# Optimization experiments

Measured on AMD Instinct MI355X. Metric: run time of the kernel, lower is better.

Reference implementation:

```python
import jax, jax.numpy as jnp
import numpy as np

N_HEAD = 8
N_EMBD = 512
HEAD_DIM = N_EMBD // N_HEAD


def setup_inputs() -> dict:
    key = jax.random.key(0)
    ks = jax.random.split(key, 9)
    B, S, D = 2, 4096, N_EMBD
    scale = 1.0 / np.sqrt(D)
    x = jax.random.normal(ks[0], (B, S, D), dtype=jnp.float32)
    Wq = jax.random.normal(ks[1], (D, D), dtype=jnp.float32) * scale
    bq = jax.random.normal(ks[2], (D,), dtype=jnp.float32) * 0.01
    Wk = jax.random.normal(ks[3], (D, D), dtype=jnp.float32) * scale
    bk = jax.random.normal(ks[4], (D,), dtype=jnp.float32) * 0.01
    Wv = jax.random.normal(ks[5], (D, D), dtype=jnp.float32) * scale
    bv = jax.random.normal(ks[6], (D,), dtype=jnp.float32) * 0.01
    Wo = jax.random.normal(ks[7], (D, D), dtype=jnp.float32) * scale
    bo = jax.random.normal(ks[8], (D,), dtype=jnp.float32) * 0.01
    return {"x": x, "Wq": Wq, "bq": bq, "Wk": Wk, "bk": bk,
            "Wv": Wv, "bv": bv, "Wo": Wo, "bo": bo}


def reference(x, Wq, bq, Wk, bk, Wv, bv, Wo, bo):
    B, S, D = x.shape
    H, Hd = N_HEAD, HEAD_DIM
    q = (x @ Wq + bq).reshape(B, S, H, Hd)
    k = (x @ Wk + bk).reshape(B, S, H, Hd)
    v = (x @ Wv + bv).reshape(B, S, H, Hd)
    # scores: [B, H, S, S]
    scores = jnp.einsum('bqhd,bkhd->bhqk', q, k) / jnp.sqrt(jnp.asarray(Hd, x.dtype))
    attn = jax.nn.softmax(scores, axis=-1)
    out = jnp.einsum('bhqk,bkhd->bqhd', attn, v).reshape(B, S, D)
    return out @ Wo + bo
```

## Files before the change

kernel.cpp:

```cpp
#include <hip/hip_runtime.h>

#define DEV static __device__ __forceinline__

using f32x4 = __attribute__((ext_vector_type(4))) float;
using s16x8 = __attribute__((ext_vector_type(8))) short;

DEV unsigned short f2bf(float x) {
    unsigned int u = __float_as_uint(x);
    unsigned int r = (u + 0x7FFFu + ((u >> 16) & 1u)) >> 16;
    return (unsigned short)r;
}
DEV float bf2f(unsigned short u) {
    return __uint_as_float(((unsigned int)u) << 16);
}

DEV f32x4 mfma16(s16x8 a, s16x8 b, f32x4 c) {
    return __builtin_amdgcn_mfma_f32_16x16x32_bf16(a, b, c, 0, 0, 0);
}

DEV unsigned cvtpk_bf16(float a, float b) {
    unsigned r;
    asm volatile("v_cvt_pk_bf16_f32 %0, %1, %2" : "=v"(r) : "v"(a), "v"(b));
    return r;
}

DEV void gload16(const unsigned short* g, short* l) {
    __builtin_amdgcn_global_load_lds(
        (const __attribute__((address_space(1))) unsigned int*)g,
        (__attribute__((address_space(3))) unsigned int*)l, 16, 0, 0);
}

#define LOG2E 1.4426950408889634f

__global__ void k_split(const float* __restrict__ in, unsigned short* __restrict__ hi,
                        unsigned short* __restrict__ lo, int n4) {
    for (int i = blockIdx.x * blockDim.x + threadIdx.x; i < n4; i += gridDim.x * blockDim.x) {
        float4 v = ((const float4*)in)[i];
        ushort4 h, l;
        h.x = f2bf(v.x); l.x = f2bf(v.x - bf2f(h.x));
        h.y = f2bf(v.y); l.y = f2bf(v.y - bf2f(h.y));
        h.z = f2bf(v.z); l.z = f2bf(v.z - bf2f(h.z));
        h.w = f2bf(v.w); l.w = f2bf(v.w - bf2f(h.w));
        ((ushort4*)hi)[i] = h;
        ((ushort4*)lo)[i] = l;
    }
}

__global__ void k_wfuse(const float* __restrict__ Wq, const float* __restrict__ Wk,
                        const float* __restrict__ Wv, const float* __restrict__ Wo,
                        const float* __restrict__ bq, const float* __restrict__ bk,
                        const float* __restrict__ bv,
                        unsigned short* __restrict__ WBhi, unsigned short* __restrict__ WBlo,
                        unsigned short* __restrict__ Wothi, unsigned short* __restrict__ Wotlo,
                        float* __restrict__ bcat, float qs) {
    __shared__ float tile[64][65];
    int blk = blockIdx.x;
    if (blk >= 256) {
        int i = (blk - 256) * 256 + threadIdx.x;
        bcat[i] = (i < 512) ? bq[i] * qs : (i < 1024) ? bk[i - 512] : bv[i - 1024];
        return;
    }
    int wi = blk >> 6, sub = blk & 63;
    const float* W = (wi == 0) ? Wq : (wi == 1) ? Wk : (wi == 2) ? Wv : Wo;
    float scale = (wi == 0) ? qs : 1.0f;
    unsigned short* Thi = (wi < 3) ? WBhi + (size_t)wi * 512 * 512 : Wothi;
    unsigned short* Tlo = (wi < 3) ? WBlo + (size_t)wi * 512 * 512 : Wotlo;
    int bk0 = (sub >> 3) * 64, bn = (sub & 7) * 64;
    int t = threadIdx.x;
    int r = t >> 2, c4 = (t & 3) * 16;
#pragma unroll
    for (int j = 0; j < 16; j += 4) {
        float4 v = *(const float4*)&W[(size_t)(bk0 + r) * 512 + bn + c4 + j];
        tile[r][c4 + j + 0] = v.x; tile[r][c4 + j + 1] = v.y;
        tile[r][c4 + j + 2] = v.z; tile[r][c4 + j + 3] = v.w;
    }
    __syncthreads();
    int n = t >> 2, k4 = (t & 3) * 16;
#pragma unroll
    for (int j = 0; j < 16; ++j) {
        float x = tile[k4 + j][n] * scale;
        unsigned short h = f2bf(x);
        Thi[(size_t)(bn + n) * 512 + bk0 + k4 + j] = h;
        Tlo[(size_t)(bn + n) * 512 + bk0 + k4 + j] = f2bf(x - bf2f(h));
    }
}

template <int MODE>
__global__ __launch_bounds__(256, 2) void k_gemm2(
    const unsigned short* __restrict__ Ahi, const unsigned short* __restrict__ Alo,
    const unsigned short* __restrict__ Bhi, const unsigned short* __restrict__ Blo,
    const float* __restrict__ bias,
    unsigned short* __restrict__ Qh,
    unsigned short* __restrict__ Kh, unsigned short* __restrict__ Kl,
    unsigned short* __restrict__ Vt,
    float* __restrict__ Cf) {
    __shared__ short As[128 * 64];
    __shared__ short Bs[128 * 64];
    int t = threadIdx.x, lane = t & 63, w = t >> 6;
    int wr = w >> 1, wc = w & 1, lr = lane & 15, lg = lane >> 4;
    int bm = blockIdx.y * 128, bn = blockIdx.x * 128;
    f32x4 acc[4][4] = {};
    int srow = t >> 3;
    int sc = t & 7;
    int gcol = (sc ^ (srow & 7)) * 8;
    int axr = (lr & 7) * 8;
    for (int c = 0; c < 24; ++c) {
        int seg = c >> 3, kb = (c & 7) * 64;
        const unsigned short* Ap = (seg < 2) ? Ahi : Alo;
        const unsigned short* Bp = (seg == 1) ? Blo : Bhi;
        const unsigned short* ag = Ap + (size_t)(bm + srow) * 512 + kb + gcol;
        const unsigned short* bg = Bp + (size_t)(bn + srow) * 512 + kb + gcol;
#pragma unroll
        for (int ps = 0; ps < 4; ++ps) {
            gload16(ag + (size_t)ps * 32 * 512, &As[(srow + ps * 32) * 64 + sc * 8]);
            gload16(bg + (size_t)ps * 32 * 512, &Bs[(srow + ps * 32) * 64 + sc * 8]);
        }
        __syncthreads();
#pragma unroll
        for (int kk = 0; kk < 2; ++kk) {
            s16x8 af[4], bf[4];
#pragma unroll
            for (int i = 0; i < 4; ++i)
                af[i] = *(const s16x8*)&As[(wr * 64 + i * 16 + lr) * 64 + ((kk * 32 + lg * 8) ^ axr)];
#pragma unroll
            for (int i = 0; i < 4; ++i)
                bf[i] = *(const s16x8*)&Bs[(wc * 64 + i * 16 + lr) * 64 + ((kk * 32 + lg * 8) ^ axr)];
#pragma unroll
            for (int i = 0; i < 4; ++i)
#pragma unroll
                for (int j = 0; j < 4; ++j) acc[i][j] = mfma16(af[i], bf[j], acc[i][j]);
        }
        __syncthreads();
    }
    int sel = bn >> 9;
#pragma unroll
    for (int i = 0; i < 4; ++i)
#pragma unroll
        for (int j = 0; j < 4; ++j) {
            int m = bm + wr * 64 + i * 16 + lg * 4;
            int n0 = bn + wc * 64 + j * 16;
            float bv = bias[n0 + lr];
            if (MODE == 1) {
#pragma unroll
                for (int r = 0; r < 4; ++r)
                    Cf[(size_t)(m + r) * 512 + n0 + lr] = acc[i][j][r] + bv;
            } else if (sel == 0) {
                int col = (n0 & 511) + lr;
#pragma unroll
                for (int r = 0; r < 4; ++r)
                    Qh[(size_t)(m + r) * 512 + col] = f2bf(acc[i][j][r] + bv);
            } else if (sel == 1) {
                int col = (n0 & 511) + lr;
#pragma unroll
                for (int r = 0; r < 4; ++r) {
                    float v = acc[i][j][r] + bv;
                    unsigned short hh = f2bf(v);
                    Kh[(size_t)(m + r) * 512 + col] = hh;
                    Kl[(size_t)(m + r) * 512 + col] = f2bf(v - bf2f(hh));
                }
            } else {
                int nc = (n0 & 511) + lr;
                int bidx = m >> 12, s = m & 4095;
                size_t row = ((size_t)bidx * 8 + (nc >> 6)) * 64 + (nc & 63);
                uint2 pv;
                pv.x = cvtpk_bf16(acc[i][j][0] + bv, acc[i][j][1] + bv);
                pv.y = cvtpk_bf16(acc[i][j][2] + bv, acc[i][j][3] + bv);
                *(uint2*)&Vt[row * 4096 + s] = pv;
            }
        }
}

__global__ __launch_bounds__(256, 2) void k_attn(
    const unsigned short* __restrict__ Qhi,
    const unsigned short* __restrict__ Khi, const unsigned short* __restrict__ Klo,
    const unsigned short* __restrict__ Vthi,
    unsigned short* __restrict__ Ohi, unsigned short* __restrict__ Olo) {
    __shared__ short Ks[64][136];
    __shared__ short Vs[64][72];
    __shared__ short Ps[4][2304];
    int t = threadIdx.x, lane = t & 63, w = t >> 6;
    int lr = lane & 15, lg = lane >> 4;
    int qt = blockIdx.x & 31, bh = blockIdx.x >> 5;
    int b = bh >> 3, h = bh & 7;
    int qbase = qt * 128 + w * 32;

    s16x8 qr[2][2];
#pragma unroll
    for (int qf = 0; qf < 2; ++qf) {
        size_t mrow = (size_t)(b * 4096 + qbase + qf * 16 + lr) * 512 + h * 64;
        qr[qf][0] = *(const s16x8*)&Qhi[mrow + lg * 8];
        qr[qf][1] = *(const s16x8*)&Qhi[mrow + 32 + lg * 8];
    }

    f32x4 oacc[4][2] = {};
    float mrun[2] = {-1e30f, -1e30f}, lrun[2] = {0.f, 0.f};
    short* pw = &Ps[w][0];

    int srow = t >> 2, p = t & 3;
    int db = (p & 1) * 32;
    const unsigned short* Kbase = ((p < 2) ? Khi : Klo) +
        (size_t)(b * 4096 + srow) * 512 + h * 64 + db;
    const unsigned short* Vbase = Vthi + (size_t)(bh * 64 + srow) * 4096 + p * 16;

    s16x8 kst[4], vst[2];
    {
        kst[0] = *(const s16x8*)(Kbase);      kst[1] = *(const s16x8*)(Kbase + 8);
        kst[2] = *(const s16x8*)(Kbase + 16); kst[3] = *(const s16x8*)(Kbase + 24);
        vst[0] = *(const s16x8*)(Vbase);      vst[1] = *(const s16x8*)(Vbase + 8);
    }

    for (int kt = 0; kt < 64; ++kt) {
        *(s16x8*)&Ks[srow][p * 32 + 0] = kst[0];  *(s16x8*)&Ks[srow][p * 32 + 8] = kst[1];
        *(s16x8*)&Ks[srow][p * 32 + 16] = kst[2]; *(s16x8*)&Ks[srow][p * 32 + 24] = kst[3];
        *(s16x8*)&Vs[srow][p * 16 + 0] = vst[0];  *(s16x8*)&Vs[srow][p * 16 + 8] = vst[1];
        {
            int ktn = (kt < 63) ? kt + 1 : 63;
            const unsigned short* kg = Kbase + (size_t)ktn * 64 * 512;
            const unsigned short* vg = Vbase + ktn * 64;
            kst[0] = *(const s16x8*)(kg);      kst[1] = *(const s16x8*)(kg + 8);
            kst[2] = *(const s16x8*)(kg + 16); kst[3] = *(const s16x8*)(kg + 24);
            vst[0] = *(const s16x8*)(vg);      vst[1] = *(const s16x8*)(vg + 8);
        }
        __syncthreads();

        f32x4 sacc[4][2] = {};
        __builtin_amdgcn_s_setprio(1);
#pragma unroll
        for (int kk = 0; kk < 4; ++kk) {
            int qa = kk & 1;
#pragma unroll
            for (int kf = 0; kf < 4; ++kf) {
                s16x8 af = *(const s16x8*)&Ks[kf * 16 + lr][kk * 32 + lg * 8];
                sacc[kf][0] = mfma16(af, qr[0][qa], sacc[kf][0]);
                sacc[kf][1] = mfma16(af, qr[1][qa], sacc[kf][1]);
            }
        }
        __builtin_amdgcn_s_setprio(0);

#pragma unroll
        for (int qf = 0; qf < 2; ++qf) {
            float tmax = -1e30f;
#pragma unroll
            for (int kf = 0; kf < 4; ++kf)
#pragma unroll
                for (int r = 0; r < 4; ++r) tmax = fmaxf(tmax, sacc[kf][qf][r]);
            tmax = fmaxf(tmax, __shfl_xor(tmax, 16));
            tmax = fmaxf(tmax, __shfl_xor(tmax, 32));
            if (!__all(tmax <= mrun[qf] + 4.0f)) {
                float mnew = fmaxf(mrun[qf], tmax);
                float alpha = exp2f(mrun[qf] - mnew);
                mrun[qf] = mnew;
                lrun[qf] *= alpha;
#pragma unroll
                for (int df = 0; df < 4; ++df) oacc[df][qf] *= alpha;
            }
            float m = mrun[qf];
            float tsum = 0.f;
#pragma unroll
            for (int kf = 0; kf < 4; ++kf)
#pragma unroll
                for (int r = 0; r < 4; ++r) {
                    float pv = exp2f(sacc[kf][qf][r] - m);
                    sacc[kf][qf][r] = pv;
                    tsum += pv;
                }
            tsum += __shfl_xor(tsum, 16);
            tsum += __shfl_xor(tsum, 32);
            lrun[qf] += tsum;

            int q = qf * 16 + lr;
#pragma unroll
            for (int kf = 0; kf < 4; ++kf) {
                int kcol = kf * 16 + lg * 4;
                uint2 hv;
                hv.x = cvtpk_bf16(sacc[kf][qf][0], sacc[kf][qf][1]);
                hv.y = cvtpk_bf16(sacc[kf][qf][2], sacc[kf][qf][3]);
                *(uint2*)&pw[q * 72 + kcol] = hv;
            }
        }

        s16x8 pfr[2][2];
#pragma unroll
        for (int qf = 0; qf < 2; ++qf)
#pragma unroll
            for (int pp = 0; pp < 2; ++pp)
                pfr[qf][pp] = *(const s16x8*)&pw[(qf * 16 + lr) * 72 + pp * 32 + lg * 8];
        __builtin_amdgcn_s_setprio(1);
#pragma unroll
        for (int vv = 0; vv < 2; ++vv) {
#pragma unroll
            for (int df = 0; df < 4; ++df) {
                s16x8 vf = *(const s16x8*)&Vs[df * 16 + lr][vv * 32 + lg * 8];
                oacc[df][0] = mfma16(vf, pfr[0][vv], oacc[df][0]);
                oacc[df][1] = mfma16(vf, pfr[1][vv], oacc[df][1]);
            }
        }
        __builtin_amdgcn_s_setprio(0);
        __syncthreads();
    }

    float inv0 = 1.f / lrun[0], inv1 = 1.f / lrun[1];
    float* ow = ((w < 2) ? (float*)&Ks[0][0] : (float*)&Ps[0][0]) + (w & 1) * 2176;
#pragma unroll
    for (int df = 0; df < 4; ++df) {
        f32x4 v0 = oacc[df][0] * inv0;
        f32x4 v1 = oacc[df][1] * inv1;
        *(f32x4*)&ow[(0 + lr) * 68 + df * 16 + lg * 4] = v0;
        *(f32x4*)&ow[(16 + lr) * 68 + df * 16 + lg * 4] = v1;
    }
#pragma unroll
    for (int pp = 0; pp < 2; ++pp) {
        int q = pp * 16 + (lane >> 2);
        int dc = (lane & 3) * 16;
        size_t gbase = (size_t)(b * 4096 + qbase + q) * 512 + h * 64 + dc;
        s16x8 hv0, hv1, lv0, lv1;
#pragma unroll
        for (int j = 0; j < 8; ++j) {
            float x = ow[q * 68 + dc + j];
            unsigned short hh = f2bf(x);
            hv0[j] = (short)hh; lv0[j] = (short)f2bf(x - bf2f(hh));
        }
#pragma unroll
        for (int j = 0; j < 8; ++j) {
            float x = ow[q * 68 + dc + 8 + j];
            unsigned short hh = f2bf(x);
            hv1[j] = (short)hh; lv1[j] = (short)f2bf(x - bf2f(hh));
        }
        *(s16x8*)&Ohi[gbase] = hv0;     *(s16x8*)&Ohi[gbase + 8] = hv1;
        *(s16x8*)&Olo[gbase] = lv0;     *(s16x8*)&Olo[gbase + 8] = lv1;
    }
}

extern "C" void kernel_launch(void* const* d_in, const int* in_sizes, int n_in,
                              void* d_out, int out_size, void* d_ws, size_t ws_size,
                              hipStream_t stream) {
    const float* x  = (const float*)d_in[0];
    const float* Wq = (const float*)d_in[1];
    const float* bq = (const float*)d_in[2];
    const float* Wk = (const float*)d_in[3];
    const float* bk = (const float*)d_in[4];
    const float* Wv = (const float*)d_in[5];
    const float* bv = (const float*)d_in[6];
    const float* Wo = (const float*)d_in[7];
    const float* bo = (const float*)d_in[8];
    float* out = (float*)d_out;

    char* ws = (char*)d_ws;
    const size_t PLANE = (size_t)8192 * 512 * 2;
    const size_t WBPL  = (size_t)1536 * 512 * 2;
    const size_t WPL   = (size_t)512 * 512 * 2;
    size_t off = 0;
    unsigned short* Xhi   = (unsigned short*)(ws + off); off += PLANE;
    unsigned short* Xlo   = (unsigned short*)(ws + off); off += PLANE;
    unsigned short* WBhi  = (unsigned short*)(ws + off); off += WBPL;
    unsigned short* WBlo  = (unsigned short*)(ws + off); off += WBPL;
    unsigned short* Wothi = (unsigned short*)(ws + off); off += WPL;
    unsigned short* Wotlo = (unsigned short*)(ws + off); off += WPL;
    float*          bcat  = (float*)(ws + off);          off += 1536 * 4;
    unsigned short* Qhi   = (unsigned short*)(ws + off); off += PLANE;
    unsigned short* Khi   = (unsigned short*)(ws + off); off += PLANE;
    unsigned short* Klo   = (unsigned short*)(ws + off); off += PLANE;
    unsigned short* Vthi  = (unsigned short*)(ws + off); off += PLANE;
    unsigned short* Ohi = Xhi;
    unsigned short* Olo = Xlo;

    const float QS = 0.125f * LOG2E;

    k_split<<<1024, 256, 0, stream>>>(x, Xhi, Xlo, 8192 * 512 / 4);
    k_wfuse<<<262, 256, 0, stream>>>(Wq, Wk, Wv, Wo, bq, bk, bv,
                                     WBhi, WBlo, Wothi, Wotlo, bcat, QS);
    k_gemm2<0><<<dim3(12, 64), 256, 0, stream>>>(Xhi, Xlo, WBhi, WBlo, bcat,
                                                 Qhi, Khi, Klo, Vthi, nullptr);
    k_attn<<<512, 256, 0, stream>>>(Qhi, Khi, Klo, Vthi, Ohi, Olo);
    k_gemm2<1><<<dim3(4, 64), 256, 0, stream>>>(Ohi, Olo, Wothi, Wotlo, bo,
                                                nullptr, nullptr, nullptr, nullptr, out);
}
```

Measured before the change: 322.2 us.

## Split attention across 8 waves with 16 queries each and raise occupancy

The attention kernel now runs 512 threads per block, with 8 waves each owning 16 query rows instead of 4 waves owning 32. K/V staging is spread over more threads, and shared memory is laid out as one flat buffer holding the K, V and per-wave P tiles. The aim is more waves in flight and lower register pressure per wave to hide latency. The cost is that each loaded K/V tile is reused by fewer MFMAs per wave, so the block has more LDS reads and synchronisation relative to its math. The GEMM launch bound is also raised to 3 blocks per CU.

```diff
diff --git a/kernel.cpp b/kernel.cpp
--- a/kernel.cpp
+++ b/kernel.cpp
@@ -86,7 +86,7 @@
 }
 
 template <int MODE>
-__global__ __launch_bounds__(256, 2) void k_gemm2(
+__global__ __launch_bounds__(256, 3) void k_gemm2(
     const unsigned short* __restrict__ Ahi, const unsigned short* __restrict__ Alo,
     const unsigned short* __restrict__ Bhi, const unsigned short* __restrict__ Blo,
     const float* __restrict__ bias,
@@ -170,147 +170,130 @@
         }
 }
 
-__global__ __launch_bounds__(256, 2) void k_attn(
+__global__ __launch_bounds__(512, 4) void k_attn(
     const unsigned short* __restrict__ Qhi,
     const unsigned short* __restrict__ Khi, const unsigned short* __restrict__ Klo,
     const unsigned short* __restrict__ Vthi,
     unsigned short* __restrict__ Ohi, unsigned short* __restrict__ Olo) {
-    __shared__ short Ks[64][136];
-    __shared__ short Vs[64][72];
-    __shared__ short Ps[4][2304];
+    __shared__ short L[22528];
+    short* Kls = &L[0];
+    short* Vls = &L[8704];
     int t = threadIdx.x, lane = t & 63, w = t >> 6;
     int lr = lane & 15, lg = lane >> 4;
     int qt = blockIdx.x & 31, bh = blockIdx.x >> 5;
     int b = bh >> 3, h = bh & 7;
-    int qbase = qt * 128 + w * 32;
-
-    s16x8 qr[2][2];
-#pragma unroll
-    for (int qf = 0; qf < 2; ++qf) {
-        size_t mrow = (size_t)(b * 4096 + qbase + qf * 16 + lr) * 512 + h * 64;
-        qr[qf][0] = *(const s16x8*)&Qhi[mrow + lg * 8];
-        qr[qf][1] = *(const s16x8*)&Qhi[mrow + 32 + lg * 8];
-    }
-
-    f32x4 oacc[4][2] = {};
-    float mrun[2] = {-1e30f, -1e30f}, lrun[2] = {0.f, 0.f};
-    short* pw = &Ps[w][0];
-
-    int srow = t >> 2, p = t & 3;
-    int db = (p & 1) * 32;
-    const unsigned short* Kbase = ((p < 2) ? Khi : Klo) +
-        (size_t)(b * 4096 + srow) * 512 + h * 64 + db;
-    const unsigned short* Vbase = Vthi + (size_t)(bh * 64 + srow) * 4096 + p * 16;
-
-    s16x8 kst[4], vst[2];
+    int qbase = qt * 128 + w * 16;
+    short* pw = &L[13312 + w * 1152];
+
+    s16x8 qr[2];
     {
-        kst[0] = *(const s16x8*)(Kbase);      kst[1] = *(const s16x8*)(Kbase + 8);
-        kst[2] = *(const s16x8*)(Kbase + 16); kst[3] = *(const s16x8*)(Kbase + 24);
-        vst[0] = *(const s16x8*)(Vbase);      vst[1] = *(const s16x8*)(Vbase + 8);
-    }
+        size_t mrow = (size_t)(b * 4096 + qbase + lr) * 512 + h * 64;
+        qr[0] = *(const s16x8*)&Qhi[mrow + lg * 8];
+        qr[1] = *(const s16x8*)&Qhi[mrow + 32 + lg * 8];
+    }
+
+    f32x4 oacc[4] = {};
+    float mrun = -1e30f, lrun = 0.f;
+
+    int krow = t >> 3, kp = t & 7;
+    const unsigned short* Kb = ((kp & 4) ? Klo : Khi) +
+        (size_t)(b * 4096 + krow) * 512 + h * 64 + (kp & 3) * 16;
+    int vc = (t & 7) * 8;
+    const unsigned short* Vb = Vthi + (size_t)(bh * 64 + krow) * 4096 + vc;
+
+    s16x8 k0, k1, v0;
+    k0 = *(const s16x8*)(Kb); k1 = *(const s16x8*)(Kb + 8);
+    v0 = *(const s16x8*)(Vb);
 
     for (int kt = 0; kt < 64; ++kt) {
-        *(s16x8*)&Ks[srow][p * 32 + 0] = kst[0];  *(s16x8*)&Ks[srow][p * 32 + 8] = kst[1];
-        *(s16x8*)&Ks[srow][p * 32 + 16] = kst[2]; *(s16x8*)&Ks[srow][p * 32 + 24] = kst[3];
-        *(s16x8*)&Vs[srow][p * 16 + 0] = vst[0];  *(s16x8*)&Vs[srow][p * 16 + 8] = vst[1];
+        *(s16x8*)&Kls[krow * 136 + kp * 16] = k0;
+        *(s16x8*)&Kls[krow * 136 + kp * 16 + 8] = k1;
+        *(s16x8*)&Vls[krow * 72 + vc] = v0;
         {
             int ktn = (kt < 63) ? kt + 1 : 63;
-            const unsigned short* kg = Kbase + (size_t)ktn * 64 * 512;
-            const unsigned short* vg = Vbase + ktn * 64;
-            kst[0] = *(const s16x8*)(kg);      kst[1] = *(const s16x8*)(kg + 8);
-            kst[2] = *(const s16x8*)(kg + 16); kst[3] = *(const s16x8*)(kg + 24);
-            vst[0] = *(const s16x8*)(vg);      vst[1] = *(const s16x8*)(vg + 8);
+            const unsigned short* kg = Kb + (size_t)ktn * 64 * 512;
+            const unsigned short* vg = Vb + ktn * 64;
+            k0 = *(const s16x8*)(kg); k1 = *(const s16x8*)(kg + 8);
+            v0 = *(const s16x8*)(vg);
         }
         __syncthreads();
 
-        f32x4 sacc[4][2] = {};
+        f32x4 sacc[4] = {};
         __builtin_amdgcn_s_setprio(1);
 #pragma unroll
         for (int kk = 0; kk < 4; ++kk) {
             int qa = kk & 1;
 #pragma unroll
             for (int kf = 0; kf < 4; ++kf) {
-                s16x8 af = *(const s16x8*)&Ks[kf * 16 + lr][kk * 32 + lg * 8];
-                sacc[kf][0] = mfma16(af, qr[0][qa], sacc[kf][0]);
-                sacc[kf][1] = mfma16(af, qr[1][qa], sacc[kf][1]);
+                s16x8 af = *(const s16x8*)&Kls[(kf * 16 + lr) * 136 + kk * 32 + lg * 8];
+                sacc[kf] = mfma16(af, qr[qa], sacc[kf]);
             }
         }
         __builtin_amdgcn_s_setprio(0);
 
-#pragma unroll
-        for (int qf = 0; qf < 2; ++qf) {
+        {
             float tmax = -1e30f;
 #pragma unroll
             for (int kf = 0; kf < 4; ++kf)
 #pragma unroll
-                for (int r = 0; r < 4; ++r) tmax = fmaxf(tmax, sacc[kf][qf][r]);
+                for (int r = 0; r < 4; ++r) tmax = fmaxf(tmax, sacc[kf][r]);
             tmax = fmaxf(tmax, __shfl_xor(tmax, 16));
             tmax = fmaxf(tmax, __shfl_xor(tmax, 32));
-            if (!__all(tmax <= mrun[qf] + 4.0f)) {
-                float mnew = fmaxf(mrun[qf], tmax);
-                float alpha = exp2f(mrun[qf] - mnew);
-                mrun[qf] = mnew;
-                lrun[qf] *= alpha;
-#pragma unroll
-                for (int df = 0; df < 4; ++df) oacc[df][qf] *= alpha;
-            }
-            float m = mrun[qf];
+            if (!__all(tmax <= mrun + 4.0f)) {
+                float mnew = fmaxf(mrun, tmax);
+                float alpha = exp2f(mrun - mnew);
+                mrun = mnew;
+                lrun *= alpha;
+#pragma unroll
+                for (int df = 0; df < 4; ++df) oacc[df] *= alpha;
+            }
+            float m = mrun;
             float tsum = 0.f;
 #pragma unroll
             for (int kf = 0; kf < 4; ++kf)
 #pragma unroll
                 for (int r = 0; r < 4; ++r) {
-                    float pv = exp2f(sacc[kf][qf][r] - m);
-                    sacc[kf][qf][r] = pv;
+                    float pv = exp2f(sacc[kf][r] - m);
+                    sacc[kf][r] = pv;
                     tsum += pv;
                 }
             tsum += __shfl_xor(tsum, 16);
             tsum += __shfl_xor(tsum, 32);
-            lrun[qf] += tsum;
-
-            int q = qf * 16 + lr;
+            lrun += tsum;
 #pragma unroll
             for (int kf = 0; kf < 4; ++kf) {
-                int kcol = kf * 16 + lg * 4;
                 uint2 hv;
-                hv.x = cvtpk_bf16(sacc[kf][qf][0], sacc[kf][qf][1]);
-                hv.y = cvtpk_bf16(sacc[kf][qf][2], sacc[kf][qf][3]);
-                *(uint2*)&pw[q * 72 + kcol] = hv;
-            }
-        }
-
-        s16x8 pfr[2][2];
-#pragma unroll
-        for (int qf = 0; qf < 2; ++qf)
-#pragma unroll
-            for (int pp = 0; pp < 2; ++pp)
-                pfr[qf][pp] = *(const s16x8*)&pw[(qf * 16 + lr) * 72 + pp * 32 + lg * 8];
+                hv.x = cvtpk_bf16(sacc[kf][0], sacc[kf][1]);
+                hv.y = cvtpk_bf16(sacc[kf][2], sacc[kf][3]);
+                *(uint2*)&pw[lr * 72 + kf * 16 + lg * 4] = hv;
+            }
+        }
+
+        s16x8 pfr[2];
+        pfr[0] = *(const s16x8*)&pw[lr * 72 + lg * 8];
+        pfr[1] = *(const s16x8*)&pw[lr * 72 + 32 + lg * 8];
         __builtin_amdgcn_s_setprio(1);
 #pragma unroll
         for (int vv = 0; vv < 2; ++vv) {
 #pragma unroll
             for (int df = 0; df < 4; ++df) {
-                s16x8 vf = *(const s16x8*)&Vs[df * 16 + lr][vv * 32 + lg * 8];
-                oacc[df][0] = mfma16(vf, pfr[0][vv], oacc[df][0]);
-                oacc[df][1] = mfma16(vf, pfr[1][vv], oacc[df][1]);
+                s16x8 vf = *(const s16x8*)&Vls[(df * 16 + lr) * 72 + vv * 32 + lg * 8];
+                oacc[df] = mfma16(vf, pfr[vv], oacc[df]);
             }
         }
         __builtin_amdgcn_s_setprio(0);
         __syncthreads();
     }
 
-    float inv0 = 1.f / lrun[0], inv1 = 1.f / lrun[1];
-    float* ow = ((w < 2) ? (float*)&Ks[0][0] : (float*)&Ps[0][0]) + (w & 1) * 2176;
+    float inv = 1.f / lrun;
+    float* ow = (float*)&L[0] + w * 1088;
 #pragma unroll
     for (int df = 0; df < 4; ++df) {
-        f32x4 v0 = oacc[df][0] * inv0;
-        f32x4 v1 = oacc[df][1] * inv1;
-        *(f32x4*)&ow[(0 + lr) * 68 + df * 16 + lg * 4] = v0;
-        *(f32x4*)&ow[(16 + lr) * 68 + df * 16 + lg * 4] = v1;
-    }
-#pragma unroll
-    for (int pp = 0; pp < 2; ++pp) {
-        int q = pp * 16 + (lane >> 2);
+        f32x4 v = oacc[df] * inv;
+        *(f32x4*)&ow[lr * 68 + df * 16 + lg * 4] = v;
+    }
+    {
+        int q = lane >> 2;
         int dc = (lane & 3) * 16;
         size_t gbase = (size_t)(b * 4096 + qbase + q) * 512 + h * 64 + dc;
         s16x8 hv0, hv1, lv0, lv1;
@@ -371,7 +354,7 @@
                                      WBhi, WBlo, Wothi, Wotlo, bcat, QS);
     k_gemm2<0><<<dim3(12, 64), 256, 0, stream>>>(Xhi, Xlo, WBhi, WBlo, bcat,
                                                  Qhi, Khi, Klo, Vthi, nullptr);
-    k_attn<<<512, 256, 0, stream>>>(Qhi, Khi, Klo, Vthi, Ohi, Olo);
+    k_attn<<<512, 512, 0, stream>>>(Qhi, Khi, Klo, Vthi, Ohi, Olo);
     k_gemm2<1><<<dim3(4, 64), 256, 0, stream>>>(Ohi, Olo, Wothi, Wotlo, bo,
                                                 nullptr, nullptr, nullptr, nullptr, out);
 }
```

Result: no change. 324.3 us (+0.6%).

## Drop split-bf16 K and O planes, enlarge attention blocks to 512 threads

Applied to the files above, without the earlier changes.

Removes the hi/lo bf16 split for K and the attention output. The QK^T product now uses a single bf16 K with half the MFMA k-steps, and the output projection runs 16 chunks instead of 24. Attention blocks grow to 512 threads covering 256 queries each, with a swizzled block index, a single shared-memory buffer and a simpler epilogue. The output GEMM's launch bound goes to 3 blocks per SM. This cuts memory traffic and MFMA work in exchange for lower numerical precision, which could push error past tolerance.

```diff
diff --git a/kernel.cpp b/kernel.cpp
--- a/kernel.cpp
+++ b/kernel.cpp
@@ -86,12 +86,12 @@
 }
 
 template <int MODE>
-__global__ __launch_bounds__(256, 2) void k_gemm2(
+__global__ __launch_bounds__(256, 3) void k_gemm2(
     const unsigned short* __restrict__ Ahi, const unsigned short* __restrict__ Alo,
     const unsigned short* __restrict__ Bhi, const unsigned short* __restrict__ Blo,
     const float* __restrict__ bias,
     unsigned short* __restrict__ Qh,
-    unsigned short* __restrict__ Kh, unsigned short* __restrict__ Kl,
+    unsigned short* __restrict__ Kh,
     unsigned short* __restrict__ Vt,
     float* __restrict__ Cf) {
     __shared__ short As[128 * 64];
@@ -104,10 +104,17 @@
     int sc = t & 7;
     int gcol = (sc ^ (srow & 7)) * 8;
     int axr = (lr & 7) * 8;
-    for (int c = 0; c < 24; ++c) {
+    const int NC = (MODE == 0) ? 24 : 16;
+    for (int c = 0; c < NC; ++c) {
         int seg = c >> 3, kb = (c & 7) * 64;
-        const unsigned short* Ap = (seg < 2) ? Ahi : Alo;
-        const unsigned short* Bp = (seg == 1) ? Blo : Bhi;
+        const unsigned short* Ap, * Bp;
+        if (MODE == 0) {
+            Ap = (seg < 2) ? Ahi : Alo;
+            Bp = (seg == 1) ? Blo : Bhi;
+        } else {
+            Ap = Ahi;
+            Bp = seg ? Blo : Bhi;
+        }
         const unsigned short* ag = Ap + (size_t)(bm + srow) * 512 + kb + gcol;
         const unsigned short* bg = Bp + (size_t)(bn + srow) * 512 + kb + gcol;
 #pragma unroll
@@ -144,20 +151,12 @@
 #pragma unroll
                 for (int r = 0; r < 4; ++r)
                     Cf[(size_t)(m + r) * 512 + n0 + lr] = acc[i][j][r] + bv;
-            } else if (sel == 0) {
+            } else if (sel < 2) {
                 int col = (n0 & 511) + lr;
+                unsigned short* Ph = sel ? Kh : Qh;
 #pragma unroll
                 for (int r = 0; r < 4; ++r)
-                    Qh[(size_t)(m + r) * 512 + col] = f2bf(acc[i][j][r] + bv);
-            } else if (sel == 1) {
-                int col = (n0 & 511) + lr;
-#pragma unroll
-                for (int r = 0; r < 4; ++r) {
-                    float v = acc[i][j][r] + bv;
-                    unsigned short hh = f2bf(v);
-                    Kh[(size_t)(m + r) * 512 + col] = hh;
-                    Kl[(size_t)(m + r) * 512 + col] = f2bf(v - bf2f(hh));
-                }
+                    Ph[(size_t)(m + r) * 512 + col] = f2bf(acc[i][j][r] + bv);
             } else {
                 int nc = (n0 & 511) + lr;
                 int bidx = m >> 12, s = m & 4095;
@@ -170,19 +169,22 @@
         }
 }
 
-__global__ __launch_bounds__(256, 2) void k_attn(
+__global__ __launch_bounds__(512, 2) void k_attn(
     const unsigned short* __restrict__ Qhi,
-    const unsigned short* __restrict__ Khi, const unsigned short* __restrict__ Klo,
+    const unsigned short* __restrict__ Khi,
     const unsigned short* __restrict__ Vthi,
-    unsigned short* __restrict__ Ohi, unsigned short* __restrict__ Olo) {
-    __shared__ short Ks[64][136];
-    __shared__ short Vs[64][72];
-    __shared__ short Ps[4][2304];
+    unsigned short* __restrict__ Ohi) {
+    __shared__ short L[27648];
+    short* Kls = &L[0];
+    short* Vls = &L[4608];
     int t = threadIdx.x, lane = t & 63, w = t >> 6;
     int lr = lane & 15, lg = lane >> 4;
-    int qt = blockIdx.x & 31, bh = blockIdx.x >> 5;
+    int bid = blockIdx.x;
+    int swz = (bid & 7) * 32 + (bid >> 3);
+    int bh = swz >> 4, qt = swz & 15;
     int b = bh >> 3, h = bh & 7;
-    int qbase = qt * 128 + w * 32;
+    int qbase = qt * 256 + w * 32;
+    short* pw = &L[9216 + w * 2304];
 
     s16x8 qr[2][2];
 #pragma unroll
@@ -194,47 +196,33 @@
 
     f32x4 oacc[4][2] = {};
     float mrun[2] = {-1e30f, -1e30f}, lrun[2] = {0.f, 0.f};
-    short* pw = &Ps[w][0];
-
-    int srow = t >> 2, p = t & 3;
-    int db = (p & 1) * 32;
-    const unsigned short* Kbase = ((p < 2) ? Khi : Klo) +
-        (size_t)(b * 4096 + srow) * 512 + h * 64 + db;
-    const unsigned short* Vbase = Vthi + (size_t)(bh * 64 + srow) * 4096 + p * 16;
-
-    s16x8 kst[4], vst[2];
-    {
-        kst[0] = *(const s16x8*)(Kbase);      kst[1] = *(const s16x8*)(Kbase + 8);
-        kst[2] = *(const s16x8*)(Kbase + 16); kst[3] = *(const s16x8*)(Kbase + 24);
-        vst[0] = *(const s16x8*)(Vbase);      vst[1] = *(const s16x8*)(Vbase + 8);
-    }
+
+    int krow = t >> 3, kc = (t & 7) * 8;
+    const unsigned short* Kb = Khi + (size_t)(b * 4096 + krow) * 512 + h * 64 + kc;
+    const unsigned short* Vb = Vthi + (size_t)(bh * 64 + krow) * 4096 + kc;
+    s16x8 k0 = *(const s16x8*)Kb;
+    s16x8 v0 = *(const s16x8*)Vb;
 
     for (int kt = 0; kt < 64; ++kt) {
-        *(s16x8*)&Ks[srow][p * 32 + 0] = kst[0];  *(s16x8*)&Ks[srow][p * 32 + 8] = kst[1];
-        *(s16x8*)&Ks[srow][p * 32 + 16] = kst[2]; *(s16x8*)&Ks[srow][p * 32 + 24] = kst[3];
-        *(s16x8*)&Vs[srow][p * 16 + 0] = vst[0];  *(s16x8*)&Vs[srow][p * 16 + 8] = vst[1];
+        *(s16x8*)&Kls[krow * 72 + kc] = k0;
+        *(s16x8*)&Vls[krow * 72 + kc] = v0;
         {
             int ktn = (kt < 63) ? kt + 1 : 63;
-            const unsigned short* kg = Kbase + (size_t)ktn * 64 * 512;
-            const unsigned short* vg = Vbase + ktn * 64;
-            kst[0] = *(const s16x8*)(kg);      kst[1] = *(const s16x8*)(kg + 8);
-            kst[2] = *(const s16x8*)(kg + 16); kst[3] = *(const s16x8*)(kg + 24);
-            vst[0] = *(const s16x8*)(vg);      vst[1] = *(const s16x8*)(vg + 8);
+            k0 = *(const s16x8*)(Kb + (size_t)ktn * 64 * 512);
+            v0 = *(const s16x8*)(Vb + ktn * 64);
         }
         __syncthreads();
 
         f32x4 sacc[4][2] = {};
         __builtin_amdgcn_s_setprio(1);
 #pragma unroll
-        for (int kk = 0; kk < 4; ++kk) {
-            int qa = kk & 1;
+        for (int kk = 0; kk < 2; ++kk)
 #pragma unroll
             for (int kf = 0; kf < 4; ++kf) {
-                s16x8 af = *(const s16x8*)&Ks[kf * 16 + lr][kk * 32 + lg * 8];
-                sacc[kf][0] = mfma16(af, qr[0][qa], sacc[kf][0]);
-                sacc[kf][1] = mfma16(af, qr[1][qa], sacc[kf][1]);
-            }
-        }
+                s16x8 af = *(const s16x8*)&Kls[(kf * 16 + lr) * 72 + kk * 32 + lg * 8];
+                sacc[kf][0] = mfma16(af, qr[0][kk], sacc[kf][0]);
+                sacc[kf][1] = mfma16(af, qr[1][kk], sacc[kf][1]);
+            }
         __builtin_amdgcn_s_setprio(0);
 
 #pragma unroll
@@ -271,11 +259,10 @@
             int q = qf * 16 + lr;
 #pragma unroll
             for (int kf = 0; kf < 4; ++kf) {
-                int kcol = kf * 16 + lg * 4;
                 uint2 hv;
                 hv.x = cvtpk_bf16(sacc[kf][qf][0], sacc[kf][qf][1]);
                 hv.y = cvtpk_bf16(sacc[kf][qf][2], sacc[kf][qf][3]);
-                *(uint2*)&pw[q * 72 + kcol] = hv;
+                *(uint2*)&pw[q * 72 + kf * 16 + lg * 4] = hv;
             }
         }
 
@@ -283,51 +270,44 @@
 #pragma unroll
         for (int qf = 0; qf < 2; ++qf)
 #pragma unroll
-            for (int pp = 0; pp < 2; ++pp)
-                pfr[qf][pp] = *(const s16x8*)&pw[(qf * 16 + lr) * 72 + pp * 32 + lg * 8];
+            for (int vv = 0; vv < 2; ++vv)
+                pfr[qf][vv] = *(const s16x8*)&pw[(qf * 16 + lr) * 72 + vv * 32 + lg * 8];
         __builtin_amdgcn_s_setprio(1);
 #pragma unroll
-        for (int vv = 0; vv < 2; ++vv) {
+        for (int vv = 0; vv < 2; ++vv)
 #pragma unroll
             for (int df = 0; df < 4; ++df) {
-                s16x8 vf = *(const s16x8*)&Vs[df * 16 + lr][vv * 32 + lg * 8];
+                s16x8 vf = *(const s16x8*)&Vls[(df * 16 + lr) * 72 + vv * 32 + lg * 8];
                 oacc[df][0] = mfma16(vf, pfr[0][vv], oacc[df][0]);
                 oacc[df][1] = mfma16(vf, pfr[1][vv], oacc[df][1]);
             }
-        }
         __builtin_amdgcn_s_setprio(0);
         __syncthreads();
     }
 
-    float inv0 = 1.f / lrun[0], inv1 = 1.f / lrun[1];
-    float* ow = ((w < 2) ? (float*)&Ks[0][0] : (float*)&Ps[0][0]) + (w & 1) * 2176;
-#pragma unroll
-    for (int df = 0; df < 4; ++df) {
-        f32x4 v0 = oacc[df][0] * inv0;
-        f32x4 v1 = oacc[df][1] * inv1;
-        *(f32x4*)&ow[(0 + lr) * 68 + df * 16 + lg * 4] = v0;
-        *(f32x4*)&ow[(16 + lr) * 68 + df * 16 + lg * 4] = v1;
-    }
+    float inv[2] = {1.f / lrun[0], 1.f / lrun[1]};
+    float* ow = (float*)&L[0] + w * 1088;
 #pragma unroll
     for (int pp = 0; pp < 2; ++pp) {
-        int q = pp * 16 + (lane >> 2);
-        int dc = (lane & 3) * 16;
-        size_t gbase = (size_t)(b * 4096 + qbase + q) * 512 + h * 64 + dc;
-        s16x8 hv0, hv1, lv0, lv1;
-#pragma unroll
-        for (int j = 0; j < 8; ++j) {
-            float x = ow[q * 68 + dc + j];
-            unsigned short hh = f2bf(x);
-            hv0[j] = (short)hh; lv0[j] = (short)f2bf(x - bf2f(hh));
-        }
-#pragma unroll
-        for (int j = 0; j < 8; ++j) {
-            float x = ow[q * 68 + dc + 8 + j];
-            unsigned short hh = f2bf(x);
-            hv1[j] = (short)hh; lv1[j] = (short)f2bf(x - bf2f(hh));
-        }
-        *(s16x8*)&Ohi[gbase] = hv0;     *(s16x8*)&Ohi[gbase + 8] = hv1;
-        *(s16x8*)&Olo[gbase] = lv0;     *(s16x8*)&Olo[gbase + 8] = lv1;
+        if (pp) __syncthreads();
+#pragma unroll
+        for (int df = 0; df < 4; ++df) {
+            f32x4 v = oacc[df][pp] * inv[pp];
+            *(f32x4*)&ow[lr * 68 + df * 16 + lg * 4] = v;
+        }
+        int q = lane >> 2, dc = (lane & 3) * 16;
+        f32x4 x0 = *(f32x4*)&ow[q * 68 + dc];
+        f32x4 x1 = *(f32x4*)&ow[q * 68 + dc + 4];
+        f32x4 x2 = *(f32x4*)&ow[q * 68 + dc + 8];
+        f32x4 x3 = *(f32x4*)&ow[q * 68 + dc + 12];
+        uint4 h0, h1;
+        h0.x = cvtpk_bf16(x0[0], x0[1]); h0.y = cvtpk_bf16(x0[2], x0[3]);
+        h0.z = cvtpk_bf16(x1[0], x1[1]); h0.w = cvtpk_bf16(x1[2], x1[3]);
+        h1.x = cvtpk_bf16(x2[0], x2[1]); h1.y = cvtpk_bf16(x2[2], x2[3]);
+        h1.z = cvtpk_bf16(x3[0], x3[1]); h1.w = cvtpk_bf16(x3[2], x3[3]);
+        size_t gbase = (size_t)(b * 4096 + qbase + pp * 16 + q) * 512 + h * 64 + dc;
+        *(uint4*)&Ohi[gbase] = h0;
+        *(uint4*)&Ohi[gbase + 8] = h1;
     }
 }
 
@@ -359,10 +339,8 @@
     float*          bcat  = (float*)(ws + off);          off += 1536 * 4;
     unsigned short* Qhi   = (unsigned short*)(ws + off); off += PLANE;
     unsigned short* Khi   = (unsigned short*)(ws + off); off += PLANE;
-    unsigned short* Klo   = (unsigned short*)(ws + off); off += PLANE;
     unsigned short* Vthi  = (unsigned short*)(ws + off); off += PLANE;
     unsigned short* Ohi = Xhi;
-    unsigned short* Olo = Xlo;
 
     const float QS = 0.125f * LOG2E;
 
@@ -370,8 +348,8 @@
     k_wfuse<<<262, 256, 0, stream>>>(Wq, Wk, Wv, Wo, bq, bk, bv,
                                      WBhi, WBlo, Wothi, Wotlo, bcat, QS);
     k_gemm2<0><<<dim3(12, 64), 256, 0, stream>>>(Xhi, Xlo, WBhi, WBlo, bcat,
-                                                 Qhi, Khi, Klo, Vthi, nullptr);
-    k_attn<<<512, 256, 0, stream>>>(Qhi, Khi, Klo, Vthi, Ohi, Olo);
-    k_gemm2<1><<<dim3(4, 64), 256, 0, stream>>>(Ohi, Olo, Wothi, Wotlo, bo,
-                                                nullptr, nullptr, nullptr, nullptr, out);
-}
+                                                 Qhi, Khi, Vthi, nullptr);
+    k_attn<<<256, 512, 0, stream>>>(Qhi, Khi, Vthi, Ohi);
+    k_gemm2<1><<<dim3(4, 64), 256, 0, stream>>>(Ohi, nullptr, Wothi, Wotlo, bo,
+                                                nullptr, nullptr, nullptr, out);
+}
```

Result: faster. 312.3 us (-3.1%).
